# Kernel optimization log

Hardware: AMD Instinct MI355X
Metric: run time of the kernel (lower is better)

The kernel has to match this reference:

```python
import jax, jax.numpy as jnp
import numpy as np

N = 100_000      # nodes
E = 1_600_000    # edges
IN, H, OUT = 128, 64, 32


def _gcn_edges(edge_index, n):
    """Add self-loops and compute symmetric GCN normalization (PyG gcn_norm)."""
    src, dst = edge_index[0], edge_index[1]
    loops = jnp.arange(n, dtype=src.dtype)
    src = jnp.concatenate([src, loops])
    dst = jnp.concatenate([dst, loops])
    deg = jax.ops.segment_sum(jnp.ones_like(dst, jnp.float32), dst, num_segments=n)
    dinv = jnp.where(deg > 0, jax.lax.rsqrt(deg), 0.0)
    norm = dinv[src] * dinv[dst]          # [E+N]
    return src, dst, norm


def _gcn_conv(x, src, dst, norm, W, b, n):
    h = x @ W.T                           # dense transform [n, out]
    msg = h[src] * norm[:, None]          # gather + scale per edge
    out = jax.ops.segment_sum(msg, dst, num_segments=n)  # scatter-add
    return out + b


def setup_inputs() -> dict:
    key = jax.random.key(0)
    k1, k2, k3, k4 = jax.random.split(key, 4)
    x = jax.random.normal(k1, (N, IN), dtype=jnp.float32)
    edge_index = jax.random.randint(k2, (2, E), 0, N, dtype=jnp.int32)
    # xavier_normal_: std = sqrt(2 / (fan_in + fan_out))
    W1 = jax.random.normal(k3, (H, IN), dtype=jnp.float32) * np.sqrt(2.0 / (IN + H))
    b1 = jnp.zeros((H,), dtype=jnp.float32)
    W2 = jax.random.normal(k4, (OUT, H), dtype=jnp.float32) * np.sqrt(2.0 / (H + OUT))
    b2 = jnp.zeros((OUT,), dtype=jnp.float32)
    return {"x": x, "edge_index": edge_index, "W1": W1, "b1": b1, "W2": W2, "b2": b2}


def reference(x, edge_index, W1, b1, W2, b2):
    n = x.shape[0]
    src, dst, norm = _gcn_edges(edge_index, n)
    h = _gcn_conv(x, src, dst, norm, W1, b1, n)
    h = jax.nn.relu(h)
    out = _gcn_conv(h, src, dst, norm, W2, b2, n)
    return out
```

## Files before the change

kernel.cpp:

```cpp
#include <hip/hip_runtime.h>

#define THREADS 256
#define G1 256
#define MAXNB 4096
#define BCAP 2688

using bf16x8 = __attribute__((ext_vector_type(8))) short;
using f32x4 = __attribute__((ext_vector_type(4))) float;

static __device__ __forceinline__ unsigned short f2bf(float f) {
  unsigned u = __float_as_uint(f);
  unsigned r = (u + 0x7fff + ((u >> 16) & 1)) >> 16;
  return (unsigned short)r;
}
static __device__ __forceinline__ float bflo(unsigned w) {
  return __uint_as_float(w << 16);
}
static __device__ __forceinline__ float bfhi(unsigned w) {
  return __uint_as_float(w & 0xffff0000u);
}
static __device__ __forceinline__ unsigned pk2(float a, float b) {
  return (unsigned)f2bf(a) | ((unsigned)f2bf(b) << 16);
}


__global__ void k_scan_chunk(const int* __restrict__ cnt, int* __restrict__ rp,
                             int* __restrict__ bsum, int m) {
  __shared__ int s[256];
  int b = blockIdx.x, t = threadIdx.x;
  int base = b * 1024 + t * 4;
  int v[4];
  int sum = 0;
#pragma unroll
  for (int k = 0; k < 4; ++k) {
    int i = base + k;
    v[k] = (i < m) ? cnt[i] : 0;
    sum += v[k];
  }
  s[t] = sum;
  __syncthreads();
  int mine = sum;
  for (int off = 1; off < 256; off <<= 1) {
    int y = (t >= off) ? s[t - off] : 0;
    __syncthreads();
    s[t] += y;
    __syncthreads();
  }
  int run = s[t] - mine;
  if (t == 255) bsum[b] = s[255];
#pragma unroll
  for (int k = 0; k < 4; ++k) {
    int i = base + k;
    if (i <= m) rp[i] = run;
    run += v[k];
  }
}


__launch_bounds__(256)
__global__ void k_pcount(const int* __restrict__ dst, int* __restrict__ C, int e,
                         int NB, int chunk, unsigned* __restrict__ h1b,
                         unsigned* __restrict__ h2b, int n) {
  __shared__ int h[MAXNB];
  int blk = blockIdx.x, t = threadIdx.x;
  if (blk == 0) {
    if (t < 32) h1b[(size_t)n * 32 + t] = 0u;
    else if (t < 48) h2b[(size_t)n * 16 + (t - 32)] = 0u;
  }
  for (int i = t; i < NB; i += 256) h[i] = 0;
  __syncthreads();
  int beg = blk * chunk;
  int stop = min(e, beg + chunk);
  for (int j = beg + t; j < stop; j += 256) atomicAdd(&h[dst[j] >> 7], 1);
  __syncthreads();
  for (int i = t; i < NB; i += 256) C[i * G1 + blk] = h[i];
}

__launch_bounds__(256)
__global__ void k_partition(const int* __restrict__ src, const int* __restrict__ dst,
                            const int* __restrict__ Cs, const int* __restrict__ bsum,
                            int* __restrict__ bpack, int e, int NB, int chunk,
                            int NC) {
  __shared__ int cur[MAXNB];
  __shared__ int sb[1024];
  __shared__ int ss[256];
  int blk = blockIdx.x, t = threadIdx.x;
  {
    int b4 = t * 4;
    int v4[4];
    int sum = 0;
#pragma unroll
    for (int k = 0; k < 4; ++k) {
      int i = b4 + k;
      v4[k] = (i < NC) ? bsum[i] : 0;
      sum += v4[k];
    }
    ss[t] = sum;
    __syncthreads();
    int mine = sum;
    for (int off = 1; off < 256; off <<= 1) {
      int y = (t >= off) ? ss[t - off] : 0;
      __syncthreads();
      ss[t] += y;
      __syncthreads();
    }
    int run = ss[t] - mine;
#pragma unroll
    for (int k = 0; k < 4; ++k) {
      int i = b4 + k;
      if (i < 1024) sb[i] = run;
      run += v4[k];
    }
    __syncthreads();
  }
  for (int i = t; i < NB; i += 256) {
    int f = i * G1 + blk;
    cur[i] = Cs[f] + sb[f >> 10];
  }
  __syncthreads();
  int beg = blk * chunk;
  int stop = min(e, beg + chunk);
  for (int j = beg + t; j < stop; j += 256) {
    int d = dst[j];
    int b = d >> 7;
    int pos = atomicAdd(&cur[b], 1);
    bpack[pos] = (src[j] << 7) | (d & 127);
  }
}

__launch_bounds__(256)
__global__ void k_bucket_csr(const int* __restrict__ bpack, const int* __restrict__ Cs,
                             const int* __restrict__ bsum, int* __restrict__ rp,
                             float* __restrict__ dinv, int* __restrict__ csr_src,
                             int n, int e, int NB, int NC) {
  __shared__ int cl[128];
  __shared__ int cur[128];
  __shared__ int buf[BCAP];
  __shared__ int sb[1024];
  __shared__ int ss[256];
  int blk = blockIdx.x, t = threadIdx.x;
  {
    int b4 = t * 4;
    int v4[4];
    int sum = 0;
#pragma unroll
    for (int k = 0; k < 4; ++k) {
      int i = b4 + k;
      v4[k] = (i < NC) ? bsum[i] : 0;
      sum += v4[k];
    }
    ss[t] = sum;
    __syncthreads();
    int mine = sum;
    for (int off = 1; off < 256; off <<= 1) {
      int y = (t >= off) ? ss[t - off] : 0;
      __syncthreads();
      ss[t] += y;
      __syncthreads();
    }
    int run = ss[t] - mine;
#pragma unroll
    for (int k = 0; k < 4; ++k) {
      int i = b4 + k;
      if (i < 1024) sb[i] = run;
      run += v4[k];
    }
  }
  int fb = blk * G1;
  int base, end;
  if (t < 128) cl[t] = 0;
  __syncthreads();
  base = Cs[fb] + sb[fb >> 10];
  if (blk == NB - 1) {
    end = e;
  } else {
    int fe = (blk + 1) * G1;
    end = Cs[fe] + sb[fe >> 10];
  }
  int cnt = end - base;
  if (cnt <= BCAP) {
    for (int j = base + t; j < end; j += 256) {
      int p = bpack[j];
      buf[j - base] = p;
      atomicAdd(&cl[p & 127], 1);
    }
  } else {
    for (int j = base + t; j < end; j += 256) atomicAdd(&cl[bpack[j] & 127], 1);
  }
  __syncthreads();
  int own = (t < 128) ? cl[t] : 0;
  for (int off = 1; off < 128; off <<= 1) {
    int y = (t >= off && t < 128) ? cl[t - off] : 0;
    __syncthreads();
    if (t < 128) cl[t] += y;
    __syncthreads();
  }
  if (t < 128) {
    int excl = cl[t] - own;
    int v = (blk << 7) + t;
    if (v < n) {
      rp[v] = base + excl;
      dinv[v] = rsqrtf((float)own + 1.0f);
    }
    cur[t] = base + excl;
  }
  __syncthreads();
  if (cnt <= BCAP) {
    for (int j = t; j < cnt; j += 256) {
      int p = buf[j];
      int pos = atomicAdd(&cur[p & 127], 1);
      csr_src[pos] = p >> 7;
    }
  } else {
    for (int j = base + t; j < end; j += 256) {
      int p = bpack[j];
      int pos = atomicAdd(&cur[p & 127], 1);
      csr_src[pos] = p >> 7;
    }
  }
  if (blk == 0 && t == 0) rp[n] = e;
}


__launch_bounds__(256)
__global__ void k_gemm1(const float* __restrict__ x, const float* __restrict__ W1,
                        const float* __restrict__ dinv, unsigned short* __restrict__ h1b,
                        int n) {
  __shared__ uint4 sXb[64 * 16];
  __shared__ uint4 sWb[64 * 16];
  __shared__ __align__(16) unsigned short sOut[64 * 64];
  int t = threadIdx.x;
  const float4* x4 = (const float4*)x;
  const float4* W14 = (const float4*)W1;
  int rbase = blockIdx.x * 64;
#pragma unroll
  for (int p = 0; p < 4; ++p) {
    int q = t + 256 * p;
    int r = q >> 4, s = q & 15;
    int gr = rbase + r;
    float4 v0 = make_float4(0.f, 0.f, 0.f, 0.f), v1 = v0;
    if (gr < n) {
      v0 = x4[(size_t)gr * 32 + s * 2];
      v1 = x4[(size_t)gr * 32 + s * 2 + 1];
    }
    uint4 pk;
    pk.x = pk2(v0.x, v0.y);
    pk.y = pk2(v0.z, v0.w);
    pk.z = pk2(v1.x, v1.y);
    pk.w = pk2(v1.z, v1.w);
    sXb[r * 16 + (s ^ (r & 15))] = pk;
  }
#pragma unroll
  for (int p = 0; p < 4; ++p) {
    int q = t + 256 * p;
    int c = q >> 4, s = q & 15;
    float4 v0 = W14[c * 32 + s * 2];
    float4 v1 = W14[c * 32 + s * 2 + 1];
    uint4 pk;
    pk.x = pk2(v0.x, v0.y);
    pk.y = pk2(v0.z, v0.w);
    pk.z = pk2(v1.x, v1.y);
    pk.w = pk2(v1.z, v1.w);
    sWb[c * 16 + (s ^ (c & 15))] = pk;
  }
  __syncthreads();
  int lane = t & 63;
  int w = t >> 6;
  int l16 = lane & 15, quad = lane >> 4;
  int arow = w * 16 + l16;
  f32x4 acc0 = {0.f, 0.f, 0.f, 0.f};
  f32x4 acc1 = {0.f, 0.f, 0.f, 0.f};
  f32x4 acc2 = {0.f, 0.f, 0.f, 0.f};
  f32x4 acc3 = {0.f, 0.f, 0.f, 0.f};
#pragma unroll
  for (int kc = 0; kc < 4; ++kc) {
    int slot = kc * 4 + quad;
    uint4 ua = sXb[arow * 16 + (slot ^ (arow & 15))];
    bf16x8 a = *(bf16x8*)&ua;
    uint4 ub0 = sWb[(0 + l16) * 16 + (slot ^ l16)];
    uint4 ub1 = sWb[(16 + l16) * 16 + (slot ^ l16)];
    uint4 ub2 = sWb[(32 + l16) * 16 + (slot ^ l16)];
    uint4 ub3 = sWb[(48 + l16) * 16 + (slot ^ l16)];
    acc0 = __builtin_amdgcn_mfma_f32_16x16x32_bf16(a, *(bf16x8*)&ub0, acc0, 0, 0, 0);
    acc1 = __builtin_amdgcn_mfma_f32_16x16x32_bf16(a, *(bf16x8*)&ub1, acc1, 0, 0, 0);
    acc2 = __builtin_amdgcn_mfma_f32_16x16x32_bf16(a, *(bf16x8*)&ub2, acc2, 0, 0, 0);
    acc3 = __builtin_amdgcn_mfma_f32_16x16x32_bf16(a, *(bf16x8*)&ub3, acc3, 0, 0, 0);
  }
  float dvr[4];
#pragma unroll
  for (int r = 0; r < 4; ++r) {
    int grow = rbase + w * 16 + quad * 4 + r;
    dvr[r] = (grow < n) ? dinv[grow] : 0.f;
  }
#pragma unroll
  for (int r = 0; r < 4; ++r) {
    int rl = w * 16 + quad * 4 + r;
    sOut[rl * 64 + 0 + l16] = f2bf(acc0[r] * dvr[r]);
    sOut[rl * 64 + 16 + l16] = f2bf(acc1[r] * dvr[r]);
    sOut[rl * 64 + 32 + l16] = f2bf(acc2[r] * dvr[r]);
    sOut[rl * 64 + 48 + l16] = f2bf(acc3[r] * dvr[r]);
  }
  __syncthreads();
#pragma unroll
  for (int p = 0; p < 2; ++p) {
    int q = t + 256 * p;
    int r = q >> 3, s = q & 7;
    int gr = rbase + r;
    if (gr < n)
      *(uint4*)&h1b[(size_t)gr * 64 + s * 8] = *(uint4*)&sOut[r * 64 + s * 8];
  }
}


__launch_bounds__(256)
__global__ void k_fused(const unsigned* __restrict__ h1p, const float* __restrict__ b1,
                        const float* __restrict__ W2, const float* __restrict__ dinv,
                        const int* __restrict__ rp, const int* __restrict__ csr_src,
                        unsigned short* __restrict__ h2b, int n) {
  __shared__ uint4 sXb2[64 * 8];
  __shared__ uint4 sWb2[32 * 8];
  __shared__ __align__(16) unsigned short sOut2[64 * 32];
  int t = threadIdx.x;
  int rbase = blockIdx.x * 64;
  const uint2* h1q = (const uint2*)h1p;
  const float4* W24 = (const float4*)W2;
  const float4* b14 = (const float4*)b1;
  {
    int c = t >> 3, s2 = t & 7;
    float4 v0 = W24[c * 16 + s2 * 2];
    float4 v1 = W24[c * 16 + s2 * 2 + 1];
    uint4 pk;
    pk.x = pk2(v0.x, v0.y);
    pk.y = pk2(v0.z, v0.w);
    pk.z = pk2(v1.x, v1.y);
    pk.w = pk2(v1.z, v1.w);
    sWb2[c * 8 + (s2 ^ (c & 7))] = pk;
  }
  int f4 = t & 15;
  int rloc = t >> 4;
#pragma unroll
  for (int sub = 0; sub < 4; ++sub) {
    int r = sub * 16 + rloc;
    int v = rbase + r;
    float r0 = 0.f, r1 = 0.f, r2 = 0.f, r3 = 0.f;
    if (v < n) {
      int beg = rp[v], end = rp[v + 1];
      uint2 w0 = h1q[(size_t)v * 16 + f4];
      float acc[4][4];
#pragma unroll
      for (int k = 0; k < 4; ++k)
#pragma unroll
        for (int c = 0; c < 4; ++c) acc[k][c] = 0.f;
      acc[0][0] = bflo(w0.x);
      acc[0][1] = bfhi(w0.x);
      acc[0][2] = bflo(w0.y);
      acc[0][3] = bfhi(w0.y);
      for (int j = beg; j < end; j += 4) {
        int s[4];
#pragma unroll
        for (int k = 0; k < 4; ++k) s[k] = csr_src[j + k];
#pragma unroll
        for (int k = 1; k < 4; ++k) s[k] = (j + k < end) ? s[k] : n;
        uint2 g[4];
#pragma unroll
        for (int k = 0; k < 4; ++k) g[k] = h1q[(size_t)s[k] * 16 + f4];
#pragma unroll
        for (int k = 0; k < 4; ++k) {
          acc[k][0] += bflo(g[k].x);
          acc[k][1] += bfhi(g[k].x);
          acc[k][2] += bflo(g[k].y);
          acc[k][3] += bfhi(g[k].y);
        }
      }
      float s0 = (acc[0][0] + acc[1][0]) + (acc[2][0] + acc[3][0]);
      float s1 = (acc[0][1] + acc[1][1]) + (acc[2][1] + acc[3][1]);
      float s2 = (acc[0][2] + acc[1][2]) + (acc[2][2] + acc[3][2]);
      float s3 = (acc[0][3] + acc[1][3]) + (acc[2][3] + acc[3][3]);
      float dv = dinv[v];
      float4 bb = b14[f4];
      r0 = fmaxf(fmaf(dv, s0, bb.x), 0.f);
      r1 = fmaxf(fmaf(dv, s1, bb.y), 0.f);
      r2 = fmaxf(fmaf(dv, s2, bb.z), 0.f);
      r3 = fmaxf(fmaf(dv, s3, bb.w), 0.f);
    }
    unsigned u0 = pk2(r0, r1), u1 = pk2(r2, r3);
    unsigned* xb = (unsigned*)sXb2;
    int slot = (f4 >> 1) ^ (r & 7);
    xb[(r * 8 + slot) * 4 + (f4 & 1) * 2 + 0] = u0;
    xb[(r * 8 + slot) * 4 + (f4 & 1) * 2 + 1] = u1;
  }
  __syncthreads();
  int lane = t & 63;
  int w = t >> 6;
  int l16 = lane & 15, quad = lane >> 4;
  int arow = w * 16 + l16;
  f32x4 acc0 = {0.f, 0.f, 0.f, 0.f};
  f32x4 acc1 = {0.f, 0.f, 0.f, 0.f};
#pragma unroll
  for (int kc = 0; kc < 2; ++kc) {
    int slot = kc * 4 + quad;
    uint4 ua = sXb2[arow * 8 + (slot ^ (arow & 7))];
    bf16x8 a = *(bf16x8*)&ua;
    uint4 ub0 = sWb2[l16 * 8 + (slot ^ (l16 & 7))];
    uint4 ub1 = sWb2[(16 + l16) * 8 + (slot ^ (l16 & 7))];
    acc0 = __builtin_amdgcn_mfma_f32_16x16x32_bf16(a, *(bf16x8*)&ub0, acc0, 0, 0, 0);
    acc1 = __builtin_amdgcn_mfma_f32_16x16x32_bf16(a, *(bf16x8*)&ub1, acc1, 0, 0, 0);
  }
  float dvr[4];
#pragma unroll
  for (int r = 0; r < 4; ++r) {
    int grow = rbase + w * 16 + quad * 4 + r;
    dvr[r] = (grow < n) ? dinv[grow] : 0.f;
  }
#pragma unroll
  for (int r = 0; r < 4; ++r) {
    int rl = w * 16 + quad * 4 + r;
    sOut2[rl * 32 + l16] = f2bf(acc0[r] * dvr[r]);
    sOut2[rl * 32 + 16 + l16] = f2bf(acc1[r] * dvr[r]);
  }
  __syncthreads();
  {
    int r = t >> 2, s2 = t & 3;
    int gr = rbase + r;
    if (gr < n)
      *(uint4*)&h2b[(size_t)gr * 32 + s2 * 8] = *(uint4*)&sOut2[r * 32 + s2 * 8];
  }
}


__launch_bounds__(256)
__global__ void k_agg2(const unsigned* __restrict__ h2p, const float* __restrict__ dinv,
                       const int* __restrict__ rp, const int* __restrict__ csr_src,
                       const float* __restrict__ b2, float* __restrict__ out, int n) {
  int gid = blockIdx.x * 256 + threadIdx.x;
  int v = gid >> 3, f4 = gid & 7;
  if (v >= n) return;
  const uint2* h2q = (const uint2*)h2p;
  int beg = rp[v], end = rp[v + 1];
  uint2 w0 = h2q[(size_t)v * 8 + f4];
  float acc[8][4];
#pragma unroll
  for (int k = 0; k < 8; ++k)
#pragma unroll
    for (int c = 0; c < 4; ++c) acc[k][c] = 0.f;
  acc[0][0] = bflo(w0.x);
  acc[0][1] = bfhi(w0.x);
  acc[0][2] = bflo(w0.y);
  acc[0][3] = bfhi(w0.y);
  for (int j = beg; j < end; j += 8) {
    int s[8];
#pragma unroll
    for (int k = 0; k < 8; ++k) s[k] = csr_src[j + k];
#pragma unroll
    for (int k = 1; k < 8; ++k) s[k] = (j + k < end) ? s[k] : n;
    uint2 g[8];
#pragma unroll
    for (int k = 0; k < 8; ++k) g[k] = h2q[(size_t)s[k] * 8 + f4];
#pragma unroll
    for (int k = 0; k < 8; ++k) {
      acc[k & 3][0] += bflo(g[k].x);
      acc[k & 3][1] += bfhi(g[k].x);
      acc[k & 3][2] += bflo(g[k].y);
      acc[k & 3][3] += bfhi(g[k].y);
    }
  }
  float s0 = (acc[0][0] + acc[1][0]) + (acc[2][0] + acc[3][0]);
  float s1 = (acc[0][1] + acc[1][1]) + (acc[2][1] + acc[3][1]);
  float s2 = (acc[0][2] + acc[1][2]) + (acc[2][2] + acc[3][2]);
  float s3 = (acc[0][3] + acc[1][3]) + (acc[2][3] + acc[3][3]);
  float dv = dinv[v];
  float4 bv = ((const float4*)b2)[f4];
  float4 o;
  o.x = fmaf(dv, s0, bv.x);
  o.y = fmaf(dv, s1, bv.y);
  o.z = fmaf(dv, s2, bv.z);
  o.w = fmaf(dv, s3, bv.w);
  ((float4*)out)[(size_t)v * 8 + f4] = o;
}


extern "C" void kernel_launch(void* const* d_in, const int* in_sizes, int n_in,
                              void* d_out, int out_size, void* d_ws, size_t ws_size,
                              hipStream_t stream) {
  const float* x = (const float*)d_in[0];
  const int* ei = (const int*)d_in[1];
  const float* W1 = (const float*)d_in[2];
  const float* b1 = (const float*)d_in[3];
  const float* W2 = (const float*)d_in[4];
  const float* b2 = (const float*)d_in[5];
  float* out = (float*)d_out;

  const int n = in_sizes[0] / 128;
  const int e = in_sizes[1] / 2;
  const int* src = ei;
  const int* dst = ei + e;

  const int NB = (n + 127) >> 7;
  const int m = NB * G1;
  const int chunk = (e + G1 - 1) / G1;
  const int NC = (m + 1 + 1023) / 1024;

  char* base = (char*)d_ws;
  size_t off = 0;
  auto alloc = [&](size_t bytes) {
    char* p = base + off;
    off = (off + bytes + 255) & ~(size_t)255;
    return p;
  };
  int* C = (int*)alloc((size_t)m * 4);
  int* Cs = (int*)alloc((size_t)(m + 1) * 4);
  int* bsum = (int*)alloc(1024 * 4);
  int* bpack = (int*)alloc((size_t)e * 4);
  int* rp = (int*)alloc((size_t)(n + 1) * 4);
  int* csr_src = (int*)alloc((size_t)(e + 8) * 4);
  float* dinv = (float*)alloc((size_t)n * 4);
  unsigned short* h1b = (unsigned short*)alloc((size_t)(n + 1) * 64 * 2);
  unsigned short* h2b = (unsigned short*)alloc((size_t)(n + 1) * 32 * 2);

  k_pcount<<<G1, 256, 0, stream>>>(dst, C, e, NB, chunk, (unsigned*)h1b,
                                   (unsigned*)h2b, n);
  k_scan_chunk<<<NC, 256, 0, stream>>>(C, Cs, bsum, m);
  k_partition<<<G1, 256, 0, stream>>>(src, dst, Cs, bsum, bpack, e, NB, chunk, NC);
  k_bucket_csr<<<NB, 256, 0, stream>>>(bpack, Cs, bsum, rp, dinv, csr_src, n, e, NB,
                                       NC);

  k_gemm1<<<(n + 63) / 64, 256, 0, stream>>>(x, W1, dinv, h1b, n);
  k_fused<<<(n + 63) / 64, 256, 0, stream>>>((const unsigned*)h1b, b1, W2, dinv, rp,
                                             csr_src, h2b, n);
  {
    long long total = (long long)n * 8;
    k_agg2<<<(int)((total + 255) / 256), 256, 0, stream>>>((const unsigned*)h2b, dinv,
                                                           rp, csr_src, b2, out, n);
  }
}
```

Before: 205.2 us.

## Split hidden feature tables into 32-byte column planes for cache-friendly gathers

The bf16 hidden features h1 and h2 are stored as separate planes of 16 features (32 bytes per node) instead of full rows. The aggregation loops gather one plane at a time: four passes in the fused layer-1 kernel, and two launches of the layer-2 aggregation, one per half. Each pass touches a smaller working set that fits in cache better, at the cost of re-reading CSR indices once per plane and issuing narrower loads.

```diff
diff --git a/kernel.cpp b/kernel.cpp
--- a/kernel.cpp
+++ b/kernel.cpp
@@ -59,13 +59,19 @@
 
 __launch_bounds__(256)
 __global__ void k_pcount(const int* __restrict__ dst, int* __restrict__ C, int e,
-                         int NB, int chunk, unsigned* __restrict__ h1b,
-                         unsigned* __restrict__ h2b, int n) {
+                         int NB, int chunk, unsigned* __restrict__ h1u,
+                         unsigned* __restrict__ h2u, int n) {
   __shared__ int h[MAXNB];
   int blk = blockIdx.x, t = threadIdx.x;
   if (blk == 0) {
-    if (t < 32) h1b[(size_t)n * 32 + t] = 0u;
-    else if (t < 48) h2b[(size_t)n * 16 + (t - 32)] = 0u;
+    size_t plane = (size_t)(n + 1) * 8;
+    if (t < 32) {
+      int q = t >> 3, lane = t & 7;
+      h1u[(size_t)q * plane + (size_t)n * 8 + lane] = 0u;
+    } else if (t < 48) {
+      int hh = (t - 32) >> 3, lane = (t - 32) & 7;
+      h2u[(size_t)hh * plane + (size_t)n * 8 + lane] = 0u;
+    }
   }
   for (int i = t; i < NB; i += 256) h[i] = 0;
   __syncthreads();
@@ -224,7 +230,7 @@
 
 __launch_bounds__(256)
 __global__ void k_gemm1(const float* __restrict__ x, const float* __restrict__ W1,
-                        const float* __restrict__ dinv, unsigned short* __restrict__ h1b,
+                        const float* __restrict__ dinv, unsigned* __restrict__ h1u,
                         int n) {
   __shared__ uint4 sXb[64 * 16];
   __shared__ uint4 sWb[64 * 16];
@@ -303,28 +309,27 @@
   __syncthreads();
 #pragma unroll
   for (int p = 0; p < 2; ++p) {
-    int q = t + 256 * p;
-    int r = q >> 3, s = q & 7;
+    int q4 = t + 256 * p;
+    int r = q4 >> 3, s = q4 & 7;
     int gr = rbase + r;
     if (gr < n)
-      *(uint4*)&h1b[(size_t)gr * 64 + s * 8] = *(uint4*)&sOut[r * 64 + s * 8];
+      ((uint4*)h1u)[(size_t)(s >> 1) * (n + 1) * 2 + (size_t)gr * 2 + (s & 1)] =
+          *(uint4*)&sOut[r * 64 + s * 8];
   }
 }
 
 
 __launch_bounds__(256)
-__global__ void k_fused(const unsigned* __restrict__ h1p, const float* __restrict__ b1,
+__global__ void k_fused(const unsigned* __restrict__ h1u, const float* __restrict__ b1,
                         const float* __restrict__ W2, const float* __restrict__ dinv,
                         const int* __restrict__ rp, const int* __restrict__ csr_src,
-                        unsigned short* __restrict__ h2b, int n) {
+                        unsigned* __restrict__ h2u, int n) {
   __shared__ uint4 sXb2[64 * 8];
   __shared__ uint4 sWb2[32 * 8];
   __shared__ __align__(16) unsigned short sOut2[64 * 32];
   int t = threadIdx.x;
   int rbase = blockIdx.x * 64;
-  const uint2* h1q = (const uint2*)h1p;
   const float4* W24 = (const float4*)W2;
-  const float4* b14 = (const float4*)b1;
   {
     int c = t >> 3, s2 = t & 7;
     float4 v0 = W24[c * 16 + s2 * 2];
@@ -336,63 +341,64 @@
     pk.w = pk2(v1.z, v1.w);
     sWb2[c * 8 + (s2 ^ (c & 7))] = pk;
   }
-  int f4 = t & 15;
-  int rloc = t >> 4;
-#pragma unroll
-  for (int sub = 0; sub < 4; ++sub) {
-    int r = sub * 16 + rloc;
+  const size_t plane = (size_t)(n + 1) * 8;
+  int grp = t >> 3;
+  int lane = t & 7;
+  unsigned* xb = (unsigned*)sXb2;
+#pragma unroll
+  for (int sub = 0; sub < 2; ++sub) {
+    int r = sub * 32 + grp;
     int v = rbase + r;
-    float r0 = 0.f, r1 = 0.f, r2 = 0.f, r3 = 0.f;
+    int beg = 0, end = 0;
+    float dv = 0.f;
     if (v < n) {
-      int beg = rp[v], end = rp[v + 1];
-      uint2 w0 = h1q[(size_t)v * 16 + f4];
-      float acc[4][4];
-#pragma unroll
-      for (int k = 0; k < 4; ++k)
-#pragma unroll
-        for (int c = 0; c < 4; ++c) acc[k][c] = 0.f;
-      acc[0][0] = bflo(w0.x);
-      acc[0][1] = bfhi(w0.x);
-      acc[0][2] = bflo(w0.y);
-      acc[0][3] = bfhi(w0.y);
+      beg = rp[v];
+      end = rp[v + 1];
+      dv = dinv[v];
+    }
+#pragma unroll
+    for (int q = 0; q < 4; ++q) {
+      const unsigned* hq = h1u + (size_t)q * plane;
+      float a0[4], a1[4];
+#pragma unroll
+      for (int k = 0; k < 4; ++k) {
+        a0[k] = 0.f;
+        a1[k] = 0.f;
+      }
+      if (v < n) {
+        unsigned w0 = hq[(size_t)v * 8 + lane];
+        a0[0] = bflo(w0);
+        a1[0] = bfhi(w0);
+      }
       for (int j = beg; j < end; j += 4) {
-        int s[4];
-#pragma unroll
-        for (int k = 0; k < 4; ++k) s[k] = csr_src[j + k];
-#pragma unroll
-        for (int k = 1; k < 4; ++k) s[k] = (j + k < end) ? s[k] : n;
-        uint2 g[4];
-#pragma unroll
-        for (int k = 0; k < 4; ++k) g[k] = h1q[(size_t)s[k] * 16 + f4];
+        int s4[4];
+#pragma unroll
+        for (int k = 0; k < 4; ++k) s4[k] = csr_src[j + k];
+#pragma unroll
+        for (int k = 1; k < 4; ++k) s4[k] = (j + k < end) ? s4[k] : n;
+        unsigned g[4];
+#pragma unroll
+        for (int k = 0; k < 4; ++k) g[k] = hq[(size_t)s4[k] * 8 + lane];
 #pragma unroll
         for (int k = 0; k < 4; ++k) {
-          acc[k][0] += bflo(g[k].x);
-          acc[k][1] += bfhi(g[k].x);
-          acc[k][2] += bflo(g[k].y);
-          acc[k][3] += bfhi(g[k].y);
+          a0[k] += bflo(g[k]);
+          a1[k] += bfhi(g[k]);
         }
       }
-      float s0 = (acc[0][0] + acc[1][0]) + (acc[2][0] + acc[3][0]);
-      float s1 = (acc[0][1] + acc[1][1]) + (acc[2][1] + acc[3][1]);
-      float s2 = (acc[0][2] + acc[1][2]) + (acc[2][2] + acc[3][2]);
-      float s3 = (acc[0][3] + acc[1][3]) + (acc[2][3] + acc[3][3]);
-      float dv = dinv[v];
-      float4 bb = b14[f4];
-      r0 = fmaxf(fmaf(dv, s0, bb.x), 0.f);
-      r1 = fmaxf(fmaf(dv, s1, bb.y), 0.f);
-      r2 = fmaxf(fmaf(dv, s2, bb.z), 0.f);
-      r3 = fmaxf(fmaf(dv, s3, bb.w), 0.f);
-    }
-    unsigned u0 = pk2(r0, r1), u1 = pk2(r2, r3);
-    unsigned* xb = (unsigned*)sXb2;
-    int slot = (f4 >> 1) ^ (r & 7);
-    xb[(r * 8 + slot) * 4 + (f4 & 1) * 2 + 0] = u0;
-    xb[(r * 8 + slot) * 4 + (f4 & 1) * 2 + 1] = u1;
-  }
-  __syncthreads();
-  int lane = t & 63;
+      float sx = (a0[0] + a0[1]) + (a0[2] + a0[3]);
+      float sy = (a1[0] + a1[1]) + (a1[2] + a1[3]);
+      float2 bb = *(const float2*)&b1[q * 16 + lane * 2];
+      float r0 = fmaxf(fmaf(dv, sx, bb.x), 0.f);
+      float r1 = fmaxf(fmaf(dv, sy, bb.y), 0.f);
+      unsigned u = pk2(r0, r1);
+      int ui = 8 * q + lane;
+      xb[(r * 8 + ((ui >> 2) ^ (r & 7))) * 4 + (ui & 3)] = u;
+    }
+  }
+  __syncthreads();
+  int lane64 = t & 63;
   int w = t >> 6;
-  int l16 = lane & 15, quad = lane >> 4;
+  int l16 = lane64 & 15, quad = lane64 >> 4;
   int arow = w * 16 + l16;
   f32x4 acc0 = {0.f, 0.f, 0.f, 0.f};
   f32x4 acc1 = {0.f, 0.f, 0.f, 0.f};
@@ -423,59 +429,54 @@
     int r = t >> 2, s2 = t & 3;
     int gr = rbase + r;
     if (gr < n)
-      *(uint4*)&h2b[(size_t)gr * 32 + s2 * 8] = *(uint4*)&sOut2[r * 32 + s2 * 8];
+      ((uint4*)h2u)[(size_t)(s2 >> 1) * (n + 1) * 2 + (size_t)gr * 2 + (s2 & 1)] =
+          *(uint4*)&sOut2[r * 32 + s2 * 8];
   }
 }
 
 
 __launch_bounds__(256)
-__global__ void k_agg2(const unsigned* __restrict__ h2p, const float* __restrict__ dinv,
+__global__ void k_agg2(const unsigned* __restrict__ h2u, const float* __restrict__ dinv,
                        const int* __restrict__ rp, const int* __restrict__ csr_src,
-                       const float* __restrict__ b2, float* __restrict__ out, int n) {
+                       const float* __restrict__ b2, float* __restrict__ out, int n,
+                       int half) {
   int gid = blockIdx.x * 256 + threadIdx.x;
-  int v = gid >> 3, f4 = gid & 7;
+  int v = gid >> 3, lane = gid & 7;
   if (v >= n) return;
-  const uint2* h2q = (const uint2*)h2p;
+  const unsigned* hh = h2u + (size_t)half * (n + 1) * 8;
   int beg = rp[v], end = rp[v + 1];
-  uint2 w0 = h2q[(size_t)v * 8 + f4];
-  float acc[8][4];
-#pragma unroll
-  for (int k = 0; k < 8; ++k)
-#pragma unroll
-    for (int c = 0; c < 4; ++c) acc[k][c] = 0.f;
-  acc[0][0] = bflo(w0.x);
-  acc[0][1] = bfhi(w0.x);
-  acc[0][2] = bflo(w0.y);
-  acc[0][3] = bfhi(w0.y);
-  for (int j = beg; j < end; j += 8) {
-    int s[8];
-#pragma unroll
-    for (int k = 0; k < 8; ++k) s[k] = csr_src[j + k];
-#pragma unroll
-    for (int k = 1; k < 8; ++k) s[k] = (j + k < end) ? s[k] : n;
-    uint2 g[8];
-#pragma unroll
-    for (int k = 0; k < 8; ++k) g[k] = h2q[(size_t)s[k] * 8 + f4];
-#pragma unroll
-    for (int k = 0; k < 8; ++k) {
-      acc[k & 3][0] += bflo(g[k].x);
-      acc[k & 3][1] += bfhi(g[k].x);
-      acc[k & 3][2] += bflo(g[k].y);
-      acc[k & 3][3] += bfhi(g[k].y);
-    }
-  }
-  float s0 = (acc[0][0] + acc[1][0]) + (acc[2][0] + acc[3][0]);
-  float s1 = (acc[0][1] + acc[1][1]) + (acc[2][1] + acc[3][1]);
-  float s2 = (acc[0][2] + acc[1][2]) + (acc[2][2] + acc[3][2]);
-  float s3 = (acc[0][3] + acc[1][3]) + (acc[2][3] + acc[3][3]);
+  unsigned w0 = hh[(size_t)v * 8 + lane];
+  float a0[4], a1[4];
+#pragma unroll
+  for (int k = 0; k < 4; ++k) {
+    a0[k] = 0.f;
+    a1[k] = 0.f;
+  }
+  a0[0] = bflo(w0);
+  a1[0] = bfhi(w0);
+  for (int j = beg; j < end; j += 4) {
+    int s4[4];
+#pragma unroll
+    for (int k = 0; k < 4; ++k) s4[k] = csr_src[j + k];
+#pragma unroll
+    for (int k = 1; k < 4; ++k) s4[k] = (j + k < end) ? s4[k] : n;
+    unsigned g[4];
+#pragma unroll
+    for (int k = 0; k < 4; ++k) g[k] = hh[(size_t)s4[k] * 8 + lane];
+#pragma unroll
+    for (int k = 0; k < 4; ++k) {
+      a0[k] += bflo(g[k]);
+      a1[k] += bfhi(g[k]);
+    }
+  }
+  float sx = (a0[0] + a0[1]) + (a0[2] + a0[3]);
+  float sy = (a1[0] + a1[1]) + (a1[2] + a1[3]);
   float dv = dinv[v];
-  float4 bv = ((const float4*)b2)[f4];
-  float4 o;
-  o.x = fmaf(dv, s0, bv.x);
-  o.y = fmaf(dv, s1, bv.y);
-  o.z = fmaf(dv, s2, bv.z);
-  o.w = fmaf(dv, s3, bv.w);
-  ((float4*)out)[(size_t)v * 8 + f4] = o;
+  float2 bv = *(const float2*)&b2[half * 16 + lane * 2];
+  float2 o;
+  o.x = fmaf(dv, sx, bv.x);
+  o.y = fmaf(dv, sy, bv.y);
+  *(float2*)&out[(size_t)v * 32 + half * 16 + lane * 2] = o;
 }
 
 
@@ -514,22 +515,20 @@
   int* rp = (int*)alloc((size_t)(n + 1) * 4);
   int* csr_src = (int*)alloc((size_t)(e + 8) * 4);
   float* dinv = (float*)alloc((size_t)n * 4);
-  unsigned short* h1b = (unsigned short*)alloc((size_t)(n + 1) * 64 * 2);
-  unsigned short* h2b = (unsigned short*)alloc((size_t)(n + 1) * 32 * 2);
-
-  k_pcount<<<G1, 256, 0, stream>>>(dst, C, e, NB, chunk, (unsigned*)h1b,
-                                   (unsigned*)h2b, n);
+  unsigned* h1u = (unsigned*)alloc((size_t)(n + 1) * 4 * 32);
+  unsigned* h2u = (unsigned*)alloc((size_t)(n + 1) * 2 * 32);
+
+  k_pcount<<<G1, 256, 0, stream>>>(dst, C, e, NB, chunk, h1u, h2u, n);
   k_scan_chunk<<<NC, 256, 0, stream>>>(C, Cs, bsum, m);
   k_partition<<<G1, 256, 0, stream>>>(src, dst, Cs, bsum, bpack, e, NB, chunk, NC);
   k_bucket_csr<<<NB, 256, 0, stream>>>(bpack, Cs, bsum, rp, dinv, csr_src, n, e, NB,
                                        NC);
 
-  k_gemm1<<<(n + 63) / 64, 256, 0, stream>>>(x, W1, dinv, h1b, n);
-  k_fused<<<(n + 63) / 64, 256, 0, stream>>>((const unsigned*)h1b, b1, W2, dinv, rp,
-                                             csr_src, h2b, n);
+  k_gemm1<<<(n + 63) / 64, 256, 0, stream>>>(x, W1, dinv, h1u, n);
+  k_fused<<<(n + 63) / 64, 256, 0, stream>>>(h1u, b1, W2, dinv, rp, csr_src, h2u, n);
   {
-    long long total = (long long)n * 8;
-    k_agg2<<<(int)((total + 255) / 256), 256, 0, stream>>>((const unsigned*)h2b, dinv,
-                                                           rp, csr_src, b2, out, n);
-  }
-}
+    int blocks = (int)(((long long)n * 8 + 255) / 256);
+    k_agg2<<<blocks, 256, 0, stream>>>(h2u, dinv, rp, csr_src, b2, out, n, 0);
+    k_agg2<<<blocks, 256, 0, stream>>>(h2u, dinv, rp, csr_src, b2, out, n, 1);
+  }
+}
```

Result: slower. 250.3 us (+22.0%).

## Restructure fused layer-1 aggregation to 8 lanes per node with 16-byte gathers

Applied to the files above, without the earlier changes.

The fused aggregation+GEMM2 kernel now handles 32 nodes per block instead of 64. Each node is gathered by 8 threads using 16-byte loads, with 8 edges in flight per iteration, instead of 16 threads using 8-byte loads in four sequential sub-passes. The MFMA stage is split so each of the four waves computes one 16x16 output tile, and the grid doubles. This aims to cut per-block serialisation and raise memory-level parallelism in the irregular gather. In exchange it costs more registers per thread and leaves half the threads idle during the store. The second aggregation kernel's accumulator array is also shrunk from 8 to 4 rows.

```diff
diff --git a/kernel.cpp b/kernel.cpp
--- a/kernel.cpp
+++ b/kernel.cpp
@@ -317,12 +317,12 @@
                         const float* __restrict__ W2, const float* __restrict__ dinv,
                         const int* __restrict__ rp, const int* __restrict__ csr_src,
                         unsigned short* __restrict__ h2b, int n) {
-  __shared__ uint4 sXb2[64 * 8];
+  __shared__ uint4 sXb2[32 * 8];
   __shared__ uint4 sWb2[32 * 8];
-  __shared__ __align__(16) unsigned short sOut2[64 * 32];
+  __shared__ __align__(16) unsigned short sOut2[32 * 32];
   int t = threadIdx.x;
-  int rbase = blockIdx.x * 64;
-  const uint2* h1q = (const uint2*)h1p;
+  int rbase = blockIdx.x * 32;
+  const uint4* h1q4 = (const uint4*)h1p;
   const float4* W24 = (const float4*)W2;
   const float4* b14 = (const float4*)b1;
   {
@@ -336,90 +336,97 @@
     pk.w = pk2(v1.z, v1.w);
     sWb2[c * 8 + (s2 ^ (c & 7))] = pk;
   }
-  int f4 = t & 15;
-  int rloc = t >> 4;
-#pragma unroll
-  for (int sub = 0; sub < 4; ++sub) {
-    int r = sub * 16 + rloc;
+  {
+    int r = t >> 3;
+    int lane = t & 7;
     int v = rbase + r;
-    float r0 = 0.f, r1 = 0.f, r2 = 0.f, r3 = 0.f;
+    uint4 packed = make_uint4(0u, 0u, 0u, 0u);
     if (v < n) {
       int beg = rp[v], end = rp[v + 1];
-      uint2 w0 = h1q[(size_t)v * 16 + f4];
-      float acc[4][4];
-#pragma unroll
-      for (int k = 0; k < 4; ++k)
-#pragma unroll
-        for (int c = 0; c < 4; ++c) acc[k][c] = 0.f;
-      acc[0][0] = bflo(w0.x);
-      acc[0][1] = bfhi(w0.x);
-      acc[0][2] = bflo(w0.y);
-      acc[0][3] = bfhi(w0.y);
-      for (int j = beg; j < end; j += 4) {
-        int s[4];
-#pragma unroll
-        for (int k = 0; k < 4; ++k) s[k] = csr_src[j + k];
-#pragma unroll
-        for (int k = 1; k < 4; ++k) s[k] = (j + k < end) ? s[k] : n;
-        uint2 g[4];
-#pragma unroll
-        for (int k = 0; k < 4; ++k) g[k] = h1q[(size_t)s[k] * 16 + f4];
-#pragma unroll
-        for (int k = 0; k < 4; ++k) {
-          acc[k][0] += bflo(g[k].x);
-          acc[k][1] += bfhi(g[k].x);
-          acc[k][2] += bflo(g[k].y);
-          acc[k][3] += bfhi(g[k].y);
+      float a0[2][8];
+#pragma unroll
+      for (int b = 0; b < 2; ++b)
+#pragma unroll
+        for (int i = 0; i < 8; ++i) a0[b][i] = 0.f;
+      {
+        uint4 w0 = h1q4[(size_t)v * 8 + lane];
+        a0[0][0] = bflo(w0.x);
+        a0[0][1] = bfhi(w0.x);
+        a0[0][2] = bflo(w0.y);
+        a0[0][3] = bfhi(w0.y);
+        a0[0][4] = bflo(w0.z);
+        a0[0][5] = bfhi(w0.z);
+        a0[0][6] = bflo(w0.w);
+        a0[0][7] = bfhi(w0.w);
+      }
+      for (int j = beg; j < end; j += 8) {
+        int s8[8];
+#pragma unroll
+        for (int k = 0; k < 8; ++k) s8[k] = csr_src[j + k];
+#pragma unroll
+        for (int k = 1; k < 8; ++k) s8[k] = (j + k < end) ? s8[k] : n;
+        uint4 g[8];
+#pragma unroll
+        for (int k = 0; k < 8; ++k) g[k] = h1q4[(size_t)s8[k] * 8 + lane];
+#pragma unroll
+        for (int k = 0; k < 8; ++k) {
+          a0[k & 1][0] += bflo(g[k].x);
+          a0[k & 1][1] += bfhi(g[k].x);
+          a0[k & 1][2] += bflo(g[k].y);
+          a0[k & 1][3] += bfhi(g[k].y);
+          a0[k & 1][4] += bflo(g[k].z);
+          a0[k & 1][5] += bfhi(g[k].z);
+          a0[k & 1][6] += bflo(g[k].w);
+          a0[k & 1][7] += bfhi(g[k].w);
         }
       }
-      float s0 = (acc[0][0] + acc[1][0]) + (acc[2][0] + acc[3][0]);
-      float s1 = (acc[0][1] + acc[1][1]) + (acc[2][1] + acc[3][1]);
-      float s2 = (acc[0][2] + acc[1][2]) + (acc[2][2] + acc[3][2]);
-      float s3 = (acc[0][3] + acc[1][3]) + (acc[2][3] + acc[3][3]);
       float dv = dinv[v];
-      float4 bb = b14[f4];
-      r0 = fmaxf(fmaf(dv, s0, bb.x), 0.f);
-      r1 = fmaxf(fmaf(dv, s1, bb.y), 0.f);
-      r2 = fmaxf(fmaf(dv, s2, bb.z), 0.f);
-      r3 = fmaxf(fmaf(dv, s3, bb.w), 0.f);
-    }
-    unsigned u0 = pk2(r0, r1), u1 = pk2(r2, r3);
-    unsigned* xb = (unsigned*)sXb2;
-    int slot = (f4 >> 1) ^ (r & 7);
-    xb[(r * 8 + slot) * 4 + (f4 & 1) * 2 + 0] = u0;
-    xb[(r * 8 + slot) * 4 + (f4 & 1) * 2 + 1] = u1;
-  }
-  __syncthreads();
-  int lane = t & 63;
+      float4 bb0 = b14[lane * 2];
+      float4 bb1 = b14[lane * 2 + 1];
+      float f0 = fmaxf(fmaf(dv, a0[0][0] + a0[1][0], bb0.x), 0.f);
+      float f1 = fmaxf(fmaf(dv, a0[0][1] + a0[1][1], bb0.y), 0.f);
+      float f2 = fmaxf(fmaf(dv, a0[0][2] + a0[1][2], bb0.z), 0.f);
+      float f3 = fmaxf(fmaf(dv, a0[0][3] + a0[1][3], bb0.w), 0.f);
+      float f4 = fmaxf(fmaf(dv, a0[0][4] + a0[1][4], bb1.x), 0.f);
+      float f5 = fmaxf(fmaf(dv, a0[0][5] + a0[1][5], bb1.y), 0.f);
+      float f6 = fmaxf(fmaf(dv, a0[0][6] + a0[1][6], bb1.z), 0.f);
+      float f7 = fmaxf(fmaf(dv, a0[0][7] + a0[1][7], bb1.w), 0.f);
+      packed.x = pk2(f0, f1);
+      packed.y = pk2(f2, f3);
+      packed.z = pk2(f4, f5);
+      packed.w = pk2(f6, f7);
+    }
+    sXb2[r * 8 + (lane ^ (r & 7))] = packed;
+  }
+  __syncthreads();
+  int lane64 = t & 63;
   int w = t >> 6;
-  int l16 = lane & 15, quad = lane >> 4;
-  int arow = w * 16 + l16;
-  f32x4 acc0 = {0.f, 0.f, 0.f, 0.f};
-  f32x4 acc1 = {0.f, 0.f, 0.f, 0.f};
+  int wr = w & 1, wc = w >> 1;
+  int l16 = lane64 & 15, quad = lane64 >> 4;
+  int arow = wr * 16 + l16;
+  int bcol = wc * 16 + l16;
+  f32x4 acc = {0.f, 0.f, 0.f, 0.f};
 #pragma unroll
   for (int kc = 0; kc < 2; ++kc) {
     int slot = kc * 4 + quad;
     uint4 ua = sXb2[arow * 8 + (slot ^ (arow & 7))];
-    bf16x8 a = *(bf16x8*)&ua;
-    uint4 ub0 = sWb2[l16 * 8 + (slot ^ (l16 & 7))];
-    uint4 ub1 = sWb2[(16 + l16) * 8 + (slot ^ (l16 & 7))];
-    acc0 = __builtin_amdgcn_mfma_f32_16x16x32_bf16(a, *(bf16x8*)&ub0, acc0, 0, 0, 0);
-    acc1 = __builtin_amdgcn_mfma_f32_16x16x32_bf16(a, *(bf16x8*)&ub1, acc1, 0, 0, 0);
+    uint4 ub = sWb2[bcol * 8 + (slot ^ (bcol & 7))];
+    acc = __builtin_amdgcn_mfma_f32_16x16x32_bf16(*(bf16x8*)&ua, *(bf16x8*)&ub, acc,
+                                                  0, 0, 0);
   }
   float dvr[4];
 #pragma unroll
   for (int r = 0; r < 4; ++r) {
-    int grow = rbase + w * 16 + quad * 4 + r;
+    int grow = rbase + wr * 16 + quad * 4 + r;
     dvr[r] = (grow < n) ? dinv[grow] : 0.f;
   }
 #pragma unroll
   for (int r = 0; r < 4; ++r) {
-    int rl = w * 16 + quad * 4 + r;
-    sOut2[rl * 32 + l16] = f2bf(acc0[r] * dvr[r]);
-    sOut2[rl * 32 + 16 + l16] = f2bf(acc1[r] * dvr[r]);
-  }
-  __syncthreads();
-  {
+    int rl = wr * 16 + quad * 4 + r;
+    sOut2[rl * 32 + wc * 16 + l16] = f2bf(acc[r] * dvr[r]);
+  }
+  __syncthreads();
+  if (t < 128) {
     int r = t >> 2, s2 = t & 3;
     int gr = rbase + r;
     if (gr < n)
@@ -438,9 +445,9 @@
   const uint2* h2q = (const uint2*)h2p;
   int beg = rp[v], end = rp[v + 1];
   uint2 w0 = h2q[(size_t)v * 8 + f4];
-  float acc[8][4];
-#pragma unroll
-  for (int k = 0; k < 8; ++k)
+  float acc[4][4];
+#pragma unroll
+  for (int k = 0; k < 4; ++k)
 #pragma unroll
     for (int c = 0; c < 4; ++c) acc[k][c] = 0.f;
   acc[0][0] = bflo(w0.x);
@@ -525,7 +532,7 @@
                                        NC);
 
   k_gemm1<<<(n + 63) / 64, 256, 0, stream>>>(x, W1, dinv, h1b, n);
-  k_fused<<<(n + 63) / 64, 256, 0, stream>>>((const unsigned*)h1b, b1, W2, dinv, rp,
+  k_fused<<<(n + 31) / 32, 256, 0, stream>>>((const unsigned*)h1b, b1, W2, dinv, rp,
                                              csr_src, h2b, n);
   {
     long long total = (long long)n * 8;
```

Result: no change. 205.0 us (-0.1%).
